# Kernel optimization log

Measured on AMD Instinct MI355X. Metric: run time of the kernel, lower is better.

Reference implementation:

```python
import jax, jax.numpy as jnp
import numpy as np

N_USER, N_PC, N_URL = 200000, 50000, 100000
E_USES, E_VISITS = 1000000, 1000000
H = 64
NUM_LAYERS = 2


def setup_inputs() -> dict:
    key = jax.random.key(0)
    ks = jax.random.split(key, 32)
    ki = iter(ks)

    def nrm(shape, scale=0.1):
        return jax.random.normal(next(ki), shape, dtype=jnp.float32) * scale

    inp = {
        "x_user": jax.random.normal(next(ki), (N_USER, 6), dtype=jnp.float32),
        "x_pc": jax.random.normal(next(ki), (N_PC, 4), dtype=jnp.float32),
        "x_url": jax.random.normal(next(ki), (N_URL, 3), dtype=jnp.float32),
        # edge_uses: row0 = user src ids, row1 = pc dst ids
        "edge_uses": jnp.stack([
            jax.random.randint(next(ki), (E_USES,), 0, N_USER),
            jax.random.randint(next(ki), (E_USES,), 0, N_PC),
        ]).astype(jnp.int32),
        # edge_visits: row0 = user src ids, row1 = url dst ids
        "edge_visits": jnp.stack([
            jax.random.randint(next(ki), (E_VISITS,), 0, N_USER),
            jax.random.randint(next(ki), (E_VISITS,), 0, N_URL),
        ]).astype(jnp.int32),
        # input projections (PyG Linear: y = x @ W + b)
        "Wu": nrm((6, H)), "bu": nrm((H,)),
        "Wp": nrm((4, H)), "bp": nrm((H,)),
        "Wl": nrm((3, H)), "bl": nrm((H,)),
        # per layer, per relation SAGEConv params; relation order:
        # 0: user-uses->pc, 1: pc-used_by->user, 2: user-visits->url, 3: url-visited_by->user
        "sage_l_W": nrm((NUM_LAYERS, 4, H, H)),
        "sage_l_b": nrm((NUM_LAYERS, 4, H)),
        "sage_r_W": nrm((NUM_LAYERS, 4, H, H)),
        # classifier (dropout is identity at eval)
        "cW1": nrm((H, H // 2)), "cb1": nrm((H // 2,)),
        "cW2": nrm((H // 2, 2)), "cb2": nrm((2,)),
    }
    return inp


def _sage(x_src, x_dst, src_idx, dst_idx, W_l, b_l, W_r, n_dst):
    # SAGEConv: lin_l(mean_{neighbors} x_src) + lin_r(x_dst)
    msg = x_src[src_idx]                                   # [E, H] gather
    s = jax.ops.segment_sum(msg, dst_idx, num_segments=n_dst)
    cnt = jax.ops.segment_sum(jnp.ones((src_idx.shape[0],), jnp.float32),
                              dst_idx, num_segments=n_dst)[:, None]
    mean = jnp.where(cnt > 0, s / jnp.maximum(cnt, 1.0), 0.0)
    return mean @ W_l + b_l + x_dst @ W_r


def reference(x_user, x_pc, x_url, edge_uses, edge_visits,
              Wu, bu, Wp, bp, Wl, bl,
              sage_l_W, sage_l_b, sage_r_W,
              cW1, cb1, cW2, cb2):
    hu = x_user @ Wu + bu
    hp = x_pc @ Wp + bp
    hl = x_url @ Wl + bl

    u2p_s, u2p_d = edge_uses[0], edge_uses[1]
    u2l_s, u2l_d = edge_visits[0], edge_visits[1]

    for layer in range(NUM_LAYERS):
        WL, BL, WR = sage_l_W[layer], sage_l_b[layer], sage_r_W[layer]
        new_pc = _sage(hu, hp, u2p_s, u2p_d, WL[0], BL[0], WR[0], N_PC)
        new_user = (_sage(hp, hu, u2p_d, u2p_s, WL[1], BL[1], WR[1], N_USER)
                    + _sage(hl, hu, u2l_d, u2l_s, WL[3], BL[3], WR[3], N_USER))
        new_url = _sage(hu, hl, u2l_s, u2l_d, WL[2], BL[2], WR[2], N_URL)
        hu, hp, hl = jax.nn.relu(new_user), jax.nn.relu(new_pc), jax.nn.relu(new_url)

    h = jax.nn.relu(hu @ cW1 + cb1)
    return h @ cW2 + cb2
```

## Files before the change

kernel.cpp:

```cpp
#include <hip/hip_runtime.h>

typedef __attribute__((ext_vector_type(8))) short bf16x8;
typedef __attribute__((ext_vector_type(4))) float f32x4;
typedef __attribute__((ext_vector_type(4))) int i32x4;
typedef unsigned short u16;

constexpr int NUSER = 200000;
constexpr int NPC   = 50000;
constexpr int NURL  = 100000;
constexpr int EUSES = 1000000;
constexpr int EVIS  = 1000000;
constexpr int HD    = 64;

constexpr int SB_P  = 0;
constexpr int SB_U1 = NPC;
constexpr int SB_L  = NPC + NUSER;
constexpr int SB_U2 = NPC + NUSER + NURL;
constexpr int NTOT  = NPC + NUSER + NURL + NUSER;

constexpr int CAP_P = 56;
constexpr int CAP_U = 28;
constexpr int CAP_L = 36;

constexpr int NBIN  = 128;
constexpr int NBINS = 512;

__device__ __forceinline__ int binOfP(int k) { return (k * NBIN) / NPC; }
__device__ __forceinline__ int binOfU(int k) { return (k * NBIN) / NUSER; }
__device__ __forceinline__ int binOfL(int k) { return (k * NBIN) / NURL; }

__device__ __forceinline__ u16 f2bf(float f) {
    union { float f; unsigned u; } v; v.f = f;
    unsigned r = v.u + 0x7fff + ((v.u >> 16) & 1);
    return (u16)(r >> 16);
}
__device__ __forceinline__ float bf2f(u16 b) {
    union { unsigned u; float f; } v; v.u = ((unsigned)b) << 16; return v.f;
}
__device__ __forceinline__ void acc8(float* a, uint4 v) {
    unsigned w0 = v.x, w1 = v.y, w2 = v.z, w3 = v.w;
    a[0] += bf2f((u16)(w0 & 0xffff)); a[1] += bf2f((u16)(w0 >> 16));
    a[2] += bf2f((u16)(w1 & 0xffff)); a[3] += bf2f((u16)(w1 >> 16));
    a[4] += bf2f((u16)(w2 & 0xffff)); a[5] += bf2f((u16)(w2 >> 16));
    a[6] += bf2f((u16)(w3 & 0xffff)); a[7] += bf2f((u16)(w3 >> 16));
}


__global__ __launch_bounds__(256) void proj_k(
    const float* __restrict__ x, const float* __restrict__ W,
    const float* __restrict__ b, u16* __restrict__ h,
    int n, int din)
{
    int id = blockIdx.x * 256 + threadIdx.x;
    int node = id >> 6, c = id & 63;
    if (node >= n) return;
    float acc = b[c];
    for (int k = 0; k < din; ++k)
        acc += x[node * din + k] * W[k * 64 + c];
    h[id] = f2bf(acc);
}

__global__ __launch_bounds__(256) void bin_count_k(
    const int* __restrict__ eu, const int* __restrict__ ev,
    int* __restrict__ binCnt)
{
    __shared__ int hist[NBINS];
    int tid = threadIdx.x;
    for (int i = tid; i < NBINS; i += 256) hist[i] = 0;
    __syncthreads();
    int stride = gridDim.x * 256;
    for (int e = blockIdx.x * 256 + tid; e < EUSES; e += stride) {
        int s = __builtin_nontemporal_load(eu + e);
        int d = __builtin_nontemporal_load(eu + EUSES + e);
        atomicAdd(&hist[binOfP(d)], 1);
        atomicAdd(&hist[NBIN + binOfU(s)], 1);
    }
    for (int e = blockIdx.x * 256 + tid; e < EVIS; e += stride) {
        int s = __builtin_nontemporal_load(ev + e);
        int d = __builtin_nontemporal_load(ev + EVIS + e);
        atomicAdd(&hist[2 * NBIN + binOfL(d)], 1);
        atomicAdd(&hist[3 * NBIN + binOfU(s)], 1);
    }
    __syncthreads();
    for (int i = tid; i < NBINS; i += 256)
        if (hist[i]) atomicAdd(&binCnt[i], hist[i]);
}

__global__ __launch_bounds__(256) void bin_scan_k(
    const int* __restrict__ binCnt, int* __restrict__ binBase,
    int* __restrict__ binCursor)
{
    __shared__ int lds[256];
    int t = threadIdx.x;
    int carry = 0;
    for (int base = 0; base < NBINS; base += 256) {
        int v = binCnt[base + t];
        int x = v;
        lds[t] = x; __syncthreads();
        for (int off = 1; off < 256; off <<= 1) {
            int y = (t >= off) ? lds[t - off] : 0;
            __syncthreads();
            x += y; lds[t] = x;
            __syncthreads();
        }
        int excl = carry + x - v;
        binBase[base + t] = excl;
        binCursor[base + t] = excl;
        carry += lds[255];
        __syncthreads();
    }
}

__global__ __launch_bounds__(256) void bin_scatter_k(
    const int* __restrict__ eu, const int* __restrict__ ev,
    int* __restrict__ binCursor, int2* __restrict__ binned)
{
    __shared__ int hist[NBINS];
    __shared__ int base[NBINS];
    int tid = threadIdx.x;
    for (int i = tid; i < NBINS; i += 256) hist[i] = 0;
    __syncthreads();
    int stride = gridDim.x * 256;
    for (int e = blockIdx.x * 256 + tid; e < EUSES; e += stride) {
        int s = __builtin_nontemporal_load(eu + e);
        int d = __builtin_nontemporal_load(eu + EUSES + e);
        atomicAdd(&hist[binOfP(d)], 1);
        atomicAdd(&hist[NBIN + binOfU(s)], 1);
    }
    for (int e = blockIdx.x * 256 + tid; e < EVIS; e += stride) {
        int s = __builtin_nontemporal_load(ev + e);
        int d = __builtin_nontemporal_load(ev + EVIS + e);
        atomicAdd(&hist[2 * NBIN + binOfL(d)], 1);
        atomicAdd(&hist[3 * NBIN + binOfU(s)], 1);
    }
    __syncthreads();
    for (int i = tid; i < NBINS; i += 256)
        base[i] = hist[i] ? atomicAdd(&binCursor[i], hist[i]) : 0;
    __syncthreads();
    for (int i = tid; i < NBINS; i += 256) hist[i] = 0;
    __syncthreads();
    for (int e = blockIdx.x * 256 + tid; e < EUSES; e += stride) {
        int s = __builtin_nontemporal_load(eu + e);
        int d = __builtin_nontemporal_load(eu + EUSES + e);
        int b0 = binOfP(d);
        int r0 = atomicAdd(&hist[b0], 1);
        binned[(size_t)base[b0] + r0] = make_int2(d, s);
        int b1 = NBIN + binOfU(s);
        int r1 = atomicAdd(&hist[b1], 1);
        binned[(size_t)base[b1] + r1] = make_int2(s, d);
    }
    for (int e = blockIdx.x * 256 + tid; e < EVIS; e += stride) {
        int s = __builtin_nontemporal_load(ev + e);
        int d = __builtin_nontemporal_load(ev + EVIS + e);
        int b2 = 2 * NBIN + binOfL(d);
        int r2 = atomicAdd(&hist[b2], 1);
        binned[(size_t)base[b2] + r2] = make_int2(d, s);
        int b3 = 3 * NBIN + binOfU(s);
        int r3 = atomicAdd(&hist[b3], 1);
        binned[(size_t)base[b3] + r3] = make_int2(s, d);
    }
}

__global__ __launch_bounds__(256) void bucket_build_k(
    const int2* __restrict__ binned, const int* __restrict__ binBase,
    const int* __restrict__ binCnt, int* __restrict__ deg,
    int* __restrict__ colP, int* __restrict__ colU1,
    int* __restrict__ colL, int* __restrict__ colU2)
{
    __shared__ int ldsDeg[1568];
    int bin = blockIdx.x;
    int rel = bin >> 7, sub = bin & (NBIN - 1);
    int tid = threadIdx.x;
    int range, slot0, cap;
    int* col;
    if (rel == 0)      { range = NPC;   slot0 = SB_P;  col = colP;  cap = CAP_P; }
    else if (rel == 1) { range = NUSER; slot0 = SB_U1; col = colU1; cap = CAP_U; }
    else if (rel == 2) { range = NURL;  slot0 = SB_L;  col = colL;  cap = CAP_L; }
    else               { range = NUSER; slot0 = SB_U2; col = colU2; cap = CAP_U; }
    int lo = (sub * range + NBIN - 1) / NBIN;
    int hi = ((sub + 1) * range + NBIN - 1) / NBIN;
    int nk = hi - lo;
    for (int i = tid; i < nk; i += 256) ldsDeg[i] = 0;
    __syncthreads();
    int b0 = binBase[bin], cnt = binCnt[bin];
    for (int i = tid; i < cnt; i += 256) {
        int2 kp = binned[(size_t)b0 + i];
        int r = atomicAdd(&ldsDeg[kp.x - lo], 1);
        if (r < cap) col[(size_t)kp.x * cap + r] = kp.y;
    }
    __syncthreads();
    for (int i = tid; i < nk; i += 256) deg[slot0 + lo + i] = ldsDeg[i];
}

__global__ __launch_bounds__(256) void gather_all_k(
    const u16* __restrict__ hu, const u16* __restrict__ hp,
    const u16* __restrict__ hl,
    const int* __restrict__ colP, const int* __restrict__ colU1,
    const int* __restrict__ colL, const int* __restrict__ colU2,
    const int* __restrict__ deg, u16* __restrict__ meanAll)
{
    int t = blockIdx.x * 256 + threadIdx.x;
    int slot = t >> 3;
    if (slot >= NTOT) return;
    int lane8 = (t & 7) << 3;
    const u16* hsrc;
    const int* col;
    int cap;
    if (slot < SB_U1)      { hsrc = hu; col = colP  + (size_t)(slot)         * CAP_P; cap = CAP_P; }
    else if (slot < SB_L)  { hsrc = hp; col = colU1 + (size_t)(slot - SB_U1) * CAP_U; cap = CAP_U; }
    else if (slot < SB_U2) { hsrc = hu; col = colL  + (size_t)(slot - SB_L)  * CAP_L; cap = CAP_L; }
    else                   { hsrc = hl; col = colU2 + (size_t)(slot - SB_U2) * CAP_U; cap = CAP_U; }
    int dg = deg[slot];
    int m_n = dg < cap ? dg : cap;
    float a[8] = {0.f,0.f,0.f,0.f,0.f,0.f,0.f,0.f};
    const i32x4* colv = (const i32x4*)col;
    int nb = m_n >> 2, rem = m_n & 3;
    if (m_n > 0) {
        i32x4 c = __builtin_nontemporal_load(colv);
        for (int b = 0; b < nb; ++b) {
            i32x4 cn = __builtin_nontemporal_load(colv + b + 1);
            uint4 v0 = *(const uint4*)(hsrc + (size_t)c[0] * 64 + lane8);
            uint4 v1 = *(const uint4*)(hsrc + (size_t)c[1] * 64 + lane8);
            uint4 v2 = *(const uint4*)(hsrc + (size_t)c[2] * 64 + lane8);
            uint4 v3 = *(const uint4*)(hsrc + (size_t)c[3] * 64 + lane8);
            acc8(a, v0); acc8(a, v1); acc8(a, v2); acc8(a, v3);
            c = cn;
        }
        if (rem > 0) { uint4 v = *(const uint4*)(hsrc + (size_t)c[0] * 64 + lane8); acc8(a, v); }
        if (rem > 1) { uint4 v = *(const uint4*)(hsrc + (size_t)c[1] * 64 + lane8); acc8(a, v); }
        if (rem > 2) { uint4 v = *(const uint4*)(hsrc + (size_t)c[2] * 64 + lane8); acc8(a, v); }
    }
    float inv = dg > 0 ? 1.f / (float)dg : 0.f;
    uint4 m;
    m.x = (unsigned)f2bf(a[0] * inv) | ((unsigned)f2bf(a[1] * inv) << 16);
    m.y = (unsigned)f2bf(a[2] * inv) | ((unsigned)f2bf(a[3] * inv) << 16);
    m.z = (unsigned)f2bf(a[4] * inv) | ((unsigned)f2bf(a[5] * inv) << 16);
    m.w = (unsigned)f2bf(a[6] * inv) | ((unsigned)f2bf(a[7] * inv) << 16);
    *(uint4*)(meanAll + (size_t)slot * 64 + lane8) = m;
}

__global__ __launch_bounds__(256) void btprep_k(
    const float* __restrict__ lW, const float* __restrict__ lB,
    const float* __restrict__ rW,
    u16* __restrict__ bt, float* __restrict__ bias)
{
    int idx = blockIdx.x * 256 + threadIdx.x;
    if (idx < 57344) {
        int layer = idx / 28672, rem = idx % 28672;
        size_t wb = (size_t)layer * 4 * 4096;
        int n, k, K; float val; u16* out;
        if (rem < 8192) {
            K = 128; n = rem >> 7; k = rem & 127;
            val = k < 64 ? lW[wb + 0 * 4096 + k * 64 + n]
                         : rW[wb + 0 * 4096 + (k - 64) * 64 + n];
            out = bt + (size_t)layer * 28672;
        } else if (rem < 16384) {
            int e = rem - 8192; K = 128; n = e >> 7; k = e & 127;
            val = k < 64 ? lW[wb + 2 * 4096 + k * 64 + n]
                         : rW[wb + 2 * 4096 + (k - 64) * 64 + n];
            out = bt + (size_t)layer * 28672 + 8192;
        } else {
            int e = rem - 16384; K = 192; n = e / 192; k = e % 192;
            if (k < 64)       val = lW[wb + 1 * 4096 + k * 64 + n];
            else if (k < 128) val = lW[wb + 3 * 4096 + (k - 64) * 64 + n];
            else              val = rW[wb + 1 * 4096 + (k - 128) * 64 + n]
                                  + rW[wb + 3 * 4096 + (k - 128) * 64 + n];
            out = bt + (size_t)layer * 28672 + 16384;
        }
        int byte = n * (2 * K) + 2 * k;
        byte ^= ((n & 7) << 4);
        out[byte >> 1] = f2bf(val);
    } else if (idx < 57728) {
        int i2 = idx - 57344;
        int layer = i2 / 192, r = i2 % 192, which = r / 64, c = r % 64;
        size_t bb = (size_t)layer * 4 * 64;
        float v;
        if (which == 0)      v = lB[bb + 0 * 64 + c];
        else if (which == 1) v = lB[bb + 2 * 64 + c];
        else                 v = lB[bb + 1 * 64 + c] + lB[bb + 3 * 64 + c];
        bias[(layer * 3 + which) * 64 + c] = v;
    }
}

template<int STEPS>
__global__ __launch_bounds__(256) void sage_mfma_k(
    const u16* __restrict__ src0, const u16* __restrict__ src1,
    const u16* __restrict__ src2, u16* __restrict__ hout,
    const u16* __restrict__ Bt, const float* __restrict__ bias, int n)
{
    constexpr int K = STEPS * 32;
    __shared__ u16 sB[64 * K];
    int tid = threadIdx.x;
    for (int i = tid; i < 64 * K / 8; i += 256)
        ((uint4*)sB)[i] = ((const uint4*)Bt)[i];
    __syncthreads();

    int lane = tid & 63, wave = tid >> 6;
    int row0 = blockIdx.x * 64 + wave * 16;
    int arow = row0 + (lane & 15);
    int kq = (lane >> 4) * 8;
    bool rowok = arow < n;

    const u16* srcs[3] = {src0, src1, src2};
    f32x4 acc0 = {0.f,0.f,0.f,0.f}, acc1 = acc0, acc2 = acc0, acc3 = acc0;
    f32x4* acc[4] = {&acc0, &acc1, &acc2, &acc3};

    #pragma unroll
    for (int s = 0; s < STEPS; ++s) {
        const u16* sp = srcs[s >> 1];
        int klocal = (s & 1) * 32 + kq;
        bf16x8 afrag = {0,0,0,0,0,0,0,0};
        if (rowok) afrag = *(const bf16x8*)(sp + (size_t)arow * 64 + klocal);
        int kk = s * 32 + kq;
        #pragma unroll
        for (int t = 0; t < 4; ++t) {
            int colc = t * 16 + (lane & 15);
            int byte = colc * (2 * K) + kk * 2;
            byte ^= ((colc & 7) << 4);
            bf16x8 bfrag = *(const bf16x8*)((const char*)sB + byte);
            *acc[t] = __builtin_amdgcn_mfma_f32_16x16x32_bf16(afrag, bfrag, *acc[t], 0, 0, 0);
        }
    }

    #pragma unroll
    for (int t = 0; t < 4; ++t) {
        int colc = t * 16 + (lane & 15);
        float bs = bias[colc];
        #pragma unroll
        for (int r = 0; r < 4; ++r) {
            int row = row0 + (lane >> 4) * 4 + r;
            if (row < n)
                hout[(size_t)row * 64 + colc] = f2bf(fmaxf((*acc[t])[r] + bs, 0.f));
        }
    }
}

__global__ __launch_bounds__(256) void classifier_k(
    const u16* __restrict__ hu,
    const float* __restrict__ cW1, const float* __restrict__ cb1,
    const float* __restrict__ cW2, const float* __restrict__ cb2,
    float* __restrict__ out, int n)
{
    __shared__ float sW1[64 * 32];
    __shared__ float sX[32][65];
    __shared__ float sHid[32][33];
    __shared__ float sW2[64];
    __shared__ float sb1[32];
    __shared__ float sb2[2];
    int tid = threadIdx.x;
    for (int i = tid; i < 2048; i += 256) sW1[i] = cW1[i];
    if (tid < 64) sW2[tid] = cW2[tid];
    if (tid < 32) sb1[tid] = cb1[tid];
    if (tid < 2)  sb2[tid] = cb2[tid];
    int row0 = blockIdx.x * 32;
    {
        int r = tid >> 3, k8 = (tid & 7) * 8;
        int gr = row0 + r;
        if (gr < n) {
            uint4 v = *(const uint4*)(hu + (size_t)gr * 64 + k8);
            unsigned w[4] = {v.x, v.y, v.z, v.w};
            #pragma unroll
            for (int j = 0; j < 4; ++j) {
                sX[r][k8 + 2 * j]     = bf2f((u16)(w[j] & 0xffff));
                sX[r][k8 + 2 * j + 1] = bf2f((u16)(w[j] >> 16));
            }
        } else {
            #pragma unroll
            for (int j = 0; j < 8; ++j) sX[r][k8 + j] = 0.f;
        }
    }
    __syncthreads();
    int c  = tid & 31;
    int rb = tid >> 5;
    for (int r = rb; r < 32; r += 8) {
        float acc = sb1[c];
        #pragma unroll
        for (int k = 0; k < 64; ++k) acc += sX[r][k] * sW1[k * 32 + c];
        sHid[r][c] = fmaxf(acc, 0.f);
    }
    __syncthreads();
    if (tid < 64) {
        int r = tid >> 1, j = tid & 1;
        int gr = row0 + r;
        if (gr < n) {
            float acc = sb2[j];
            #pragma unroll
            for (int k = 0; k < 32; ++k) acc += sHid[r][k] * sW2[k * 2 + j];
            out[gr * 2 + j] = acc;
        }
    }
}

extern "C" void kernel_launch(void* const* d_in, const int* in_sizes, int n_in,
                              void* d_out, int out_size, void* d_ws, size_t ws_size,
                              hipStream_t stream)
{
    const float* x_user = (const float*)d_in[0];
    const float* x_pc   = (const float*)d_in[1];
    const float* x_url  = (const float*)d_in[2];
    const int*   e_uses = (const int*)d_in[3];
    const int*   e_vis  = (const int*)d_in[4];
    const float* Wu = (const float*)d_in[5];
    const float* bu = (const float*)d_in[6];
    const float* Wp = (const float*)d_in[7];
    const float* bp = (const float*)d_in[8];
    const float* Wl = (const float*)d_in[9];
    const float* bl = (const float*)d_in[10];
    const float* sage_l_W = (const float*)d_in[11];
    const float* sage_l_b = (const float*)d_in[12];
    const float* sage_r_W = (const float*)d_in[13];
    const float* cW1 = (const float*)d_in[14];
    const float* cb1 = (const float*)d_in[15];
    const float* cW2 = (const float*)d_in[16];
    const float* cb2 = (const float*)d_in[17];
    float* out = (float*)d_out;

    char* p = (char*)d_ws;
    auto alloc = [&](size_t bytes) { char* r = p; p += (bytes + 255) & ~(size_t)255; return r; };
    u16* hu      = (u16*)alloc((size_t)NUSER * HD * 2);
    u16* hp      = (u16*)alloc((size_t)NPC * HD * 2);
    u16* hl      = (u16*)alloc((size_t)NURL * HD * 2);
    u16* meanAll = (u16*)alloc((size_t)NTOT * HD * 2);
    u16* btbuf   = (u16*)alloc((size_t)2 * 28672 * 2);
    float* biasbuf = (float*)alloc((size_t)2 * 3 * 64 * 4);
    int* deg     = (int*)alloc((size_t)NTOT * 4);
    int* colP    = (int*)alloc((size_t)NPC   * CAP_P * 4 + 64);
    int* colU1   = (int*)alloc((size_t)NUSER * CAP_U * 4 + 64);
    int* colL    = (int*)alloc((size_t)NURL  * CAP_L * 4 + 64);
    int* colU2   = (int*)alloc((size_t)NUSER * CAP_U * 4 + 64);
    int* binCnt    = (int*)alloc(NBINS * 4);
    int* binBase   = (int*)alloc(NBINS * 4);
    int* binCursor = (int*)alloc(NBINS * 4);
    int2* binned   = (int2*)alloc((size_t)2 * (EUSES + EVIS) * 8);

    u16* meanP  = meanAll + (size_t)SB_P  * HD;
    u16* meanU1 = meanAll + (size_t)SB_U1 * HD;
    u16* meanL  = meanAll + (size_t)SB_L  * HD;
    u16* meanU2 = meanAll + (size_t)SB_U2 * HD;

    hipMemsetAsync(binCnt, 0, NBINS * sizeof(int), stream);
    bin_count_k<<<256, 256, 0, stream>>>(e_uses, e_vis, binCnt);
    bin_scan_k<<<1, 256, 0, stream>>>(binCnt, binBase, binCursor);
    bin_scatter_k<<<256, 256, 0, stream>>>(e_uses, e_vis, binCursor, binned);
    bucket_build_k<<<NBINS, 256, 0, stream>>>(
        binned, binBase, binCnt, deg, colP, colU1, colL, colU2);

    btprep_k<<<(57728 + 255) / 256, 256, 0, stream>>>(
        sage_l_W, sage_l_b, sage_r_W, btbuf, biasbuf);
    proj_k<<<(NUSER * 64 + 255) / 256, 256, 0, stream>>>(x_user, Wu, bu, hu, NUSER, 6);
    proj_k<<<(NPC   * 64 + 255) / 256, 256, 0, stream>>>(x_pc,   Wp, bp, hp, NPC,   4);
    proj_k<<<(NURL  * 64 + 255) / 256, 256, 0, stream>>>(x_url,  Wl, bl, hl, NURL,  3);

    for (int layer = 0; layer < 2; ++layer) {
        const u16* btP = btbuf + (size_t)layer * 28672;
        const u16* btL = btP + 8192;
        const u16* btU = btP + 16384;
        const float* bsP = biasbuf + (layer * 3 + 0) * 64;
        const float* bsL = biasbuf + (layer * 3 + 1) * 64;
        const float* bsU = biasbuf + (layer * 3 + 2) * 64;

        gather_all_k<<<(NTOT * 8 + 255) / 256, 256, 0, stream>>>(
            hu, hp, hl, colP, colU1, colL, colU2, deg, meanAll);

        sage_mfma_k<4><<<(NPC + 63) / 64, 256, 0, stream>>>(
            meanP, hp, hp, hp, btP, bsP, NPC);
        sage_mfma_k<4><<<(NURL + 63) / 64, 256, 0, stream>>>(
            meanL, hl, hl, hl, btL, bsL, NURL);
        sage_mfma_k<6><<<(NUSER + 63) / 64, 256, 0, stream>>>(
            meanU1, meanU2, hu, hu, btU, bsU, NUSER);
    }

    classifier_k<<<(NUSER + 31) / 32, 256, 0, stream>>>(
        hu, cW1, cb1, cW2, cb2, out, NUSER);
}
```

Before: 508.5 us.

## Use per-block bin offsets to drop recount pass and unroll gather by eight

The edge binning now writes per-block histograms and runs a three-kernel scan over bin×block counts. Each scatter block then knows its exact output offsets, so the scatter kernel no longer re-reads all edges to recount before scattering. The gather loop is unrolled to eight neighbor loads per iteration, giving more memory-level parallelism, with padding on the column buffers raised to cover the wider prefetch. This adds two small scan launches and a larger count buffer in place of a second pass over 4M edge indices.

```diff
diff --git a/kernel.cpp b/kernel.cpp
--- a/kernel.cpp
+++ b/kernel.cpp
@@ -11,6 +11,7 @@
 constexpr int EUSES = 1000000;
 constexpr int EVIS  = 1000000;
 constexpr int HD    = 64;
+constexpr int ETOT2 = 2 * (EUSES + EVIS);
 
 constexpr int SB_P  = 0;
 constexpr int SB_U1 = NPC;
@@ -24,6 +25,8 @@
 
 constexpr int NBIN  = 128;
 constexpr int NBINS = 512;
+constexpr int NSCB  = 256;
+constexpr int NSCAN = NBINS * NSCB;
 
 __device__ __forceinline__ int binOfP(int k) { return (k * NBIN) / NPC; }
 __device__ __forceinline__ int binOfU(int k) { return (k * NBIN) / NUSER; }
@@ -62,7 +65,7 @@
 
 __global__ __launch_bounds__(256) void bin_count_k(
     const int* __restrict__ eu, const int* __restrict__ ev,
-    int* __restrict__ binCnt)
+    int* __restrict__ blockCnt)
 {
     __shared__ int hist[NBINS];
     int tid = threadIdx.x;
@@ -83,19 +86,42 @@
     }
     __syncthreads();
     for (int i = tid; i < NBINS; i += 256)
-        if (hist[i]) atomicAdd(&binCnt[i], hist[i]);
-}
-
-__global__ __launch_bounds__(256) void bin_scan_k(
-    const int* __restrict__ binCnt, int* __restrict__ binBase,
-    int* __restrict__ binCursor)
+        blockCnt[i * NSCB + blockIdx.x] = hist[i];
+}
+
+__global__ __launch_bounds__(256) void scanA_k(
+    const int* __restrict__ in, int* __restrict__ out,
+    int* __restrict__ bsum, int n)
+{
+    __shared__ int lds[256];
+    int b = blockIdx.x, t = threadIdx.x;
+    int base = b * 1024 + t * 4;
+    int v[4]; int s = 0;
+    #pragma unroll
+    for (int i = 0; i < 4; ++i) { v[i] = (base + i < n) ? in[base + i] : 0; s += v[i]; }
+    int x = s;
+    lds[t] = x; __syncthreads();
+    for (int off = 1; off < 256; off <<= 1) {
+        int y = (t >= off) ? lds[t - off] : 0;
+        __syncthreads();
+        x += y; lds[t] = x;
+        __syncthreads();
+    }
+    int excl = x - s;
+    #pragma unroll
+    for (int i = 0; i < 4; ++i) { if (base + i < n) out[base + i] = excl; excl += v[i]; }
+    if (t == 255) bsum[b] = x;
+}
+
+__global__ __launch_bounds__(256) void scanB_k(int* __restrict__ bsum, int nb)
 {
     __shared__ int lds[256];
     int t = threadIdx.x;
     int carry = 0;
-    for (int base = 0; base < NBINS; base += 256) {
-        int v = binCnt[base + t];
-        int x = v;
+    for (int base = 0; base < nb; base += 256) {
+        int i = base + t;
+        int s = (i < nb) ? bsum[i] : 0;
+        int x = s;
         lds[t] = x; __syncthreads();
         for (int off = 1; off < 256; off <<= 1) {
             int y = (t >= off) ? lds[t - off] : 0;
@@ -103,67 +129,59 @@
             x += y; lds[t] = x;
             __syncthreads();
         }
-        int excl = carry + x - v;
-        binBase[base + t] = excl;
-        binCursor[base + t] = excl;
-        carry += lds[255];
+        if (i < nb) bsum[i] = carry + x - s;
+        int tot = lds[255];
         __syncthreads();
-    }
+        carry += tot;
+    }
+}
+
+__global__ __launch_bounds__(256) void scanC_k(
+    int* __restrict__ out, const int* __restrict__ bsum, int n)
+{
+    int i = blockIdx.x * 256 + threadIdx.x;
+    if (i >= n) return;
+    out[i] += bsum[i >> 10];
 }
 
 __global__ __launch_bounds__(256) void bin_scatter_k(
     const int* __restrict__ eu, const int* __restrict__ ev,
-    int* __restrict__ binCursor, int2* __restrict__ binned)
-{
-    __shared__ int hist[NBINS];
+    const int* __restrict__ blockScan, int2* __restrict__ binned)
+{
     __shared__ int base[NBINS];
+    __shared__ int cur[NBINS];
     int tid = threadIdx.x;
-    for (int i = tid; i < NBINS; i += 256) hist[i] = 0;
+    for (int i = tid; i < NBINS; i += 256) {
+        base[i] = blockScan[i * NSCB + blockIdx.x];
+        cur[i] = 0;
+    }
     __syncthreads();
     int stride = gridDim.x * 256;
     for (int e = blockIdx.x * 256 + tid; e < EUSES; e += stride) {
         int s = __builtin_nontemporal_load(eu + e);
         int d = __builtin_nontemporal_load(eu + EUSES + e);
-        atomicAdd(&hist[binOfP(d)], 1);
-        atomicAdd(&hist[NBIN + binOfU(s)], 1);
-    }
-    for (int e = blockIdx.x * 256 + tid; e < EVIS; e += stride) {
-        int s = __builtin_nontemporal_load(ev + e);
-        int d = __builtin_nontemporal_load(ev + EVIS + e);
-        atomicAdd(&hist[2 * NBIN + binOfL(d)], 1);
-        atomicAdd(&hist[3 * NBIN + binOfU(s)], 1);
-    }
-    __syncthreads();
-    for (int i = tid; i < NBINS; i += 256)
-        base[i] = hist[i] ? atomicAdd(&binCursor[i], hist[i]) : 0;
-    __syncthreads();
-    for (int i = tid; i < NBINS; i += 256) hist[i] = 0;
-    __syncthreads();
-    for (int e = blockIdx.x * 256 + tid; e < EUSES; e += stride) {
-        int s = __builtin_nontemporal_load(eu + e);
-        int d = __builtin_nontemporal_load(eu + EUSES + e);
         int b0 = binOfP(d);
-        int r0 = atomicAdd(&hist[b0], 1);
+        int r0 = atomicAdd(&cur[b0], 1);
         binned[(size_t)base[b0] + r0] = make_int2(d, s);
         int b1 = NBIN + binOfU(s);
-        int r1 = atomicAdd(&hist[b1], 1);
+        int r1 = atomicAdd(&cur[b1], 1);
         binned[(size_t)base[b1] + r1] = make_int2(s, d);
     }
     for (int e = blockIdx.x * 256 + tid; e < EVIS; e += stride) {
         int s = __builtin_nontemporal_load(ev + e);
         int d = __builtin_nontemporal_load(ev + EVIS + e);
         int b2 = 2 * NBIN + binOfL(d);
-        int r2 = atomicAdd(&hist[b2], 1);
+        int r2 = atomicAdd(&cur[b2], 1);
         binned[(size_t)base[b2] + r2] = make_int2(d, s);
         int b3 = 3 * NBIN + binOfU(s);
-        int r3 = atomicAdd(&hist[b3], 1);
+        int r3 = atomicAdd(&cur[b3], 1);
         binned[(size_t)base[b3] + r3] = make_int2(s, d);
     }
 }
 
 __global__ __launch_bounds__(256) void bucket_build_k(
-    const int2* __restrict__ binned, const int* __restrict__ binBase,
-    const int* __restrict__ binCnt, int* __restrict__ deg,
+    const int2* __restrict__ binned, const int* __restrict__ blockScan,
+    int* __restrict__ deg,
     int* __restrict__ colP, int* __restrict__ colU1,
     int* __restrict__ colL, int* __restrict__ colU2)
 {
@@ -182,7 +200,9 @@
     int nk = hi - lo;
     for (int i = tid; i < nk; i += 256) ldsDeg[i] = 0;
     __syncthreads();
-    int b0 = binBase[bin], cnt = binCnt[bin];
+    int b0 = blockScan[bin * NSCB];
+    int bend = (bin == NBINS - 1) ? ETOT2 : blockScan[(bin + 1) * NSCB];
+    int cnt = bend - b0;
     for (int i = tid; i < cnt; i += 256) {
         int2 kp = binned[(size_t)b0 + i];
         int r = atomicAdd(&ldsDeg[kp.x - lo], 1);
@@ -214,21 +234,33 @@
     int m_n = dg < cap ? dg : cap;
     float a[8] = {0.f,0.f,0.f,0.f,0.f,0.f,0.f,0.f};
     const i32x4* colv = (const i32x4*)col;
-    int nb = m_n >> 2, rem = m_n & 3;
+    int nb = m_n >> 3, rem = m_n & 7;
     if (m_n > 0) {
-        i32x4 c = __builtin_nontemporal_load(colv);
+        i32x4 c0 = __builtin_nontemporal_load(colv);
+        i32x4 c1 = __builtin_nontemporal_load(colv + 1);
         for (int b = 0; b < nb; ++b) {
-            i32x4 cn = __builtin_nontemporal_load(colv + b + 1);
-            uint4 v0 = *(const uint4*)(hsrc + (size_t)c[0] * 64 + lane8);
-            uint4 v1 = *(const uint4*)(hsrc + (size_t)c[1] * 64 + lane8);
-            uint4 v2 = *(const uint4*)(hsrc + (size_t)c[2] * 64 + lane8);
-            uint4 v3 = *(const uint4*)(hsrc + (size_t)c[3] * 64 + lane8);
+            i32x4 n0 = __builtin_nontemporal_load(colv + 2 * b + 2);
+            i32x4 n1 = __builtin_nontemporal_load(colv + 2 * b + 3);
+            uint4 v0 = *(const uint4*)(hsrc + (size_t)c0[0] * 64 + lane8);
+            uint4 v1 = *(const uint4*)(hsrc + (size_t)c0[1] * 64 + lane8);
+            uint4 v2 = *(const uint4*)(hsrc + (size_t)c0[2] * 64 + lane8);
+            uint4 v3 = *(const uint4*)(hsrc + (size_t)c0[3] * 64 + lane8);
+            uint4 v4 = *(const uint4*)(hsrc + (size_t)c1[0] * 64 + lane8);
+            uint4 v5 = *(const uint4*)(hsrc + (size_t)c1[1] * 64 + lane8);
+            uint4 v6 = *(const uint4*)(hsrc + (size_t)c1[2] * 64 + lane8);
+            uint4 v7 = *(const uint4*)(hsrc + (size_t)c1[3] * 64 + lane8);
             acc8(a, v0); acc8(a, v1); acc8(a, v2); acc8(a, v3);
-            c = cn;
-        }
-        if (rem > 0) { uint4 v = *(const uint4*)(hsrc + (size_t)c[0] * 64 + lane8); acc8(a, v); }
-        if (rem > 1) { uint4 v = *(const uint4*)(hsrc + (size_t)c[1] * 64 + lane8); acc8(a, v); }
-        if (rem > 2) { uint4 v = *(const uint4*)(hsrc + (size_t)c[2] * 64 + lane8); acc8(a, v); }
+            acc8(a, v4); acc8(a, v5); acc8(a, v6); acc8(a, v7);
+            c0 = n0; c1 = n1;
+        }
+        #pragma unroll
+        for (int r = 0; r < 7; ++r) {
+            if (r < rem) {
+                int idx = r < 4 ? c0[r] : c1[r - 4];
+                uint4 v = *(const uint4*)(hsrc + (size_t)idx * 64 + lane8);
+                acc8(a, v);
+            }
+        }
     }
     float inv = dg > 0 ? 1.f / (float)dg : 0.f;
     uint4 m;
@@ -424,26 +456,27 @@
     u16* btbuf   = (u16*)alloc((size_t)2 * 28672 * 2);
     float* biasbuf = (float*)alloc((size_t)2 * 3 * 64 * 4);
     int* deg     = (int*)alloc((size_t)NTOT * 4);
-    int* colP    = (int*)alloc((size_t)NPC   * CAP_P * 4 + 64);
-    int* colU1   = (int*)alloc((size_t)NUSER * CAP_U * 4 + 64);
-    int* colL    = (int*)alloc((size_t)NURL  * CAP_L * 4 + 64);
-    int* colU2   = (int*)alloc((size_t)NUSER * CAP_U * 4 + 64);
-    int* binCnt    = (int*)alloc(NBINS * 4);
-    int* binBase   = (int*)alloc(NBINS * 4);
-    int* binCursor = (int*)alloc(NBINS * 4);
-    int2* binned   = (int2*)alloc((size_t)2 * (EUSES + EVIS) * 8);
+    int* colP    = (int*)alloc((size_t)NPC   * CAP_P * 4 + 128);
+    int* colU1   = (int*)alloc((size_t)NUSER * CAP_U * 4 + 128);
+    int* colL    = (int*)alloc((size_t)NURL  * CAP_L * 4 + 128);
+    int* colU2   = (int*)alloc((size_t)NUSER * CAP_U * 4 + 128);
+    int* blockCnt  = (int*)alloc((size_t)NSCAN * 4);
+    int* blockScan = (int*)alloc((size_t)NSCAN * 4);
+    int* bsum      = (int*)alloc((size_t)256 * 4);
+    int2* binned   = (int2*)alloc((size_t)ETOT2 * 8);
 
     u16* meanP  = meanAll + (size_t)SB_P  * HD;
     u16* meanU1 = meanAll + (size_t)SB_U1 * HD;
     u16* meanL  = meanAll + (size_t)SB_L  * HD;
     u16* meanU2 = meanAll + (size_t)SB_U2 * HD;
 
-    hipMemsetAsync(binCnt, 0, NBINS * sizeof(int), stream);
-    bin_count_k<<<256, 256, 0, stream>>>(e_uses, e_vis, binCnt);
-    bin_scan_k<<<1, 256, 0, stream>>>(binCnt, binBase, binCursor);
-    bin_scatter_k<<<256, 256, 0, stream>>>(e_uses, e_vis, binCursor, binned);
+    bin_count_k<<<NSCB, 256, 0, stream>>>(e_uses, e_vis, blockCnt);
+    scanA_k<<<NSCAN / 1024, 256, 0, stream>>>(blockCnt, blockScan, bsum, NSCAN);
+    scanB_k<<<1, 256, 0, stream>>>(bsum, NSCAN / 1024);
+    scanC_k<<<NSCAN / 256, 256, 0, stream>>>(blockScan, bsum, NSCAN);
+    bin_scatter_k<<<NSCB, 256, 0, stream>>>(e_uses, e_vis, blockScan, binned);
     bucket_build_k<<<NBINS, 256, 0, stream>>>(
-        binned, binBase, binCnt, deg, colP, colU1, colL, colU2);
+        binned, blockScan, deg, colP, colU1, colL, colU2);
 
     btprep_k<<<(57728 + 255) / 256, 256, 0, stream>>>(
         sage_l_W, sage_l_b, sage_r_W, btbuf, biasbuf);
```

Result: no change. 516.7 us (+1.6%).
